# Kernel optimization log

Hardware: AMD Instinct MI355X
Metric: run time of the kernel (lower is better)

Reference implementation:

```python
import jax, jax.numpy as jnp
import numpy as np

NUM_HEADS = 8


def setup_inputs() -> dict:
    key = jax.random.key(0)
    ks = jax.random.split(key, 5)
    B, C, H, W = 2, 256, 64, 64
    # 0.02 scaling keeps logits in a sane range so softmax is not one-hot
    return {
        "x": jax.random.normal(ks[0], (B, C, H, W), dtype=jnp.float32),
        "w_qkv": jax.random.normal(ks[1], (3 * C, C), dtype=jnp.float32) * 0.02,
        "b_qkv": jax.random.normal(ks[2], (3 * C,), dtype=jnp.float32) * 0.02,
        "w_proj": jax.random.normal(ks[3], (C, C), dtype=jnp.float32) * 0.02,
        "b_proj": jax.random.normal(ks[4], (C,), dtype=jnp.float32) * 0.02,
    }


def reference(x, w_qkv, b_qkv, w_proj, b_proj):
    B, C, H, W = x.shape
    N = H * W
    h = NUM_HEADS
    d = C // h
    # 1x1 conv == per-pixel linear: (B,C,H,W) -> (B,3C,H,W)
    qkv = jnp.einsum('oc,bchw->bohw', w_qkv, x) + b_qkv[None, :, None, None]
    qkv = qkv.reshape(B, 3, h, d, N)
    # q,k,v: (B, h, N, d)
    q = jnp.swapaxes(qkv[:, 0], -2, -1)
    k = jnp.swapaxes(qkv[:, 1], -2, -1)
    v = jnp.swapaxes(qkv[:, 2], -2, -1)
    scale = d ** (-0.5)
    attn = jax.nn.softmax(jnp.einsum('bhnd,bhmd->bhnm', q, k) * scale, axis=-1)
    out = jnp.einsum('bhnm,bhmd->bhnd', attn, v)  # (B, h, N, d)
    # faithful to torch: transpose(1,2) -> (B,N,h,d), then row-major reshape to (B,C,H,W)
    out = jnp.swapaxes(out, 1, 2).reshape(B, C, H, W)
    out = jnp.einsum('oc,bchw->bohw', w_proj, out) + b_proj[None, :, None, None]
    return out
```

## Files before the change

### kernel.cpp

```cpp
#include <hip/hip_runtime.h>
#include <hip/hip_bf16.h>


typedef __bf16 bf16;
typedef __bf16 bf16x4 __attribute__((ext_vector_type(4)));
typedef __bf16 bf16x8 __attribute__((ext_vector_type(8)));
typedef float  f32x4  __attribute__((ext_vector_type(4)));
typedef short  s16x4  __attribute__((ext_vector_type(4)));

#if __has_builtin(__builtin_amdgcn_mfma_f32_16x16x16bf16_1k)
#define HAVE_MFMA16 1
#endif

#if __has_builtin(__builtin_amdgcn_exp2f)
#define EXP2(x) __builtin_amdgcn_exp2f(x)
#else
#define EXP2(x) exp2f(x)
#endif

#define NS 4096
#define QSCALE (0.17677669529663687f * 1.4426950408889634f)

static __device__ inline unsigned pack2(float a, float b) {
  union { bf16 h[2]; unsigned u; } v;
  v.h[0] = (bf16)a; v.h[1] = (bf16)b;
  return v.u;
}

__global__ __launch_bounds__(256) void wcvt(
    const float* __restrict__ wq, const float* __restrict__ wp,
    bf16* __restrict__ wqb, bf16* __restrict__ wpb)
{
  const int bid = blockIdx.x, t = threadIdx.x;
  if (bid < 96) {
    const int i = (bid * 256 + t) * 8;
    const float sc = (i < 65536) ? QSCALE : 1.0f;
    f32x4 a = *(const f32x4*)(wq + i);
    f32x4 b = *(const f32x4*)(wq + i + 4);
    bf16x8 o;
#pragma unroll
    for (int j = 0; j < 4; j++) { o[j] = (bf16)(a[j] * sc); o[4 + j] = (bf16)(b[j] * sc); }
    *(bf16x8*)(wqb + i) = o;
  } else {
    const int i = ((bid - 96) * 256 + t) * 8;
    f32x4 a = *(const f32x4*)(wp + i);
    f32x4 b = *(const f32x4*)(wp + i + 4);
    bf16x8 o;
#pragma unroll
    for (int j = 0; j < 4; j++) { o[j] = (bf16)a[j]; o[4 + j] = (bf16)b[j]; }
    *(bf16x8*)(wpb + i) = o;
  }
}

__global__ __launch_bounds__(512) void qkv_fused(
    const float* __restrict__ x, const bf16* __restrict__ wqb,
    const float* __restrict__ bias,
    bf16* __restrict__ qbuf, bf16* __restrict__ kbuf, bf16* __restrict__ vbuf)
{
  __shared__ bf16 As[32 * 264];
  __shared__ bf16 Vt2[2][64 * 40];
  const int n0 = blockIdx.x * 32, b = blockIdx.z ? 1 : blockIdx.y;
  const int bb = blockIdx.y;
  const int t = threadIdx.x;
  const int wv = t >> 6, L = t & 63, quad = L >> 4, lb = L & 15;
  const int grp = wv >> 2, g = wv & 3;
  (void)b;

  {
    unsigned* A32 = (unsigned*)As;
    const int nj = (t & 7) * 4;
    const int cpair = t >> 3;
#pragma unroll
    for (int pass = 0; pass < 2; pass++) {
      const int c = pass * 128 + cpair * 2;
      const float* xr = x + ((size_t)(bb * 256 + c)) * NS + n0 + nj;
      f32x4 va = *(const f32x4*)xr;
      f32x4 vb = *(const f32x4*)(xr + NS);
#pragma unroll
      for (int i = 0; i < 4; i++)
        A32[(nj + i) * 132 + pass * 64 + cpair] = pack2(va[i], vb[i]);
    }
  }
  __syncthreads();

#pragma unroll
  for (int op = 0; op < 6; op++) {
    const int ot = op * 2 + grp;
    const int o = ot * 64 + g * 16 + lb;
    f32x4 acc[2] = {};
#pragma unroll
    for (int ks = 0; ks < 8; ks++) {
      const bf16x8 bfr = *(const bf16x8*)(wqb + (size_t)o * 256 + ks * 32 + quad * 8);
#pragma unroll
      for (int a = 0; a < 2; a++) {
        const bf16x8 afr = *(const bf16x8*)&As[(a * 16 + lb) * 264 + ks * 32 + quad * 8];
        acc[a] = __builtin_amdgcn_mfma_f32_16x16x32_bf16(afr, bfr, acc[a], 0, 0, 0);
      }
    }

    const int comp = ot >> 2;
    const float bv = bias[o] * (comp == 0 ? QSCALE : 1.0f);
    if (comp < 2) {
      bf16* dst = (comp == 0) ? qbuf : kbuf;
      const int hh = (o & 255) >> 5, dd = o & 31;
      const size_t base = ((size_t)bb * 8 + hh) * NS;
#pragma unroll
      for (int a = 0; a < 2; a++)
#pragma unroll
        for (int r = 0; r < 4; r++) {
          const int n = n0 + a * 16 + quad * 4 + r;
          dst[(base + n) * 32 + dd] = (bf16)(acc[a][r] + bv);
        }
    } else {
#pragma unroll
      for (int a = 0; a < 2; a++) {
        bf16x4 pk;
#pragma unroll
        for (int r = 0; r < 4; r++) pk[r] = (bf16)(acc[a][r] + bv);
        *(bf16x4*)&Vt2[grp][(g * 16 + lb) * 40 + a * 16 + quad * 4] = pk;
      }
      __syncthreads();
      {
        const int grp2 = t >> 8, u = t & 255;
        const int row = u >> 2, nc = (u & 3) * 8;
        const int ot2 = op * 2 + grp2;
        const int o2 = ot2 * 64 + row;
        const int hh2 = (o2 & 255) >> 5, dd2 = o2 & 31;
        bf16x8 v = *(const bf16x8*)&Vt2[grp2][row * 40 + nc];
        *(bf16x8*)(vbuf + (((size_t)bb * 8 + hh2) * 32 + dd2) * NS + n0 + nc) = v;
      }
      __syncthreads();
    }
  }
}

#define VT_OFF 2560
#define KV_SZ  (2560 + 32 * 72)

__global__ __launch_bounds__(512) void attn_kernel(
    const bf16* __restrict__ qbuf, const bf16* __restrict__ kbuf,
    const bf16* __restrict__ vbuf, bf16* __restrict__ abuf)
{
  __shared__ bf16 KV[2][KV_SZ];
#ifndef HAVE_MFMA16
  __shared__ bf16 Ps[8][16 * 72];
#endif

  const int qb = blockIdx.x;
  const int bh = blockIdx.y;
  const bf16* Q  = qbuf + (size_t)bh * NS * 32;
  const bf16* K  = kbuf + (size_t)bh * NS * 32;
  const bf16* Vt = vbuf + (size_t)bh * 32 * NS;

  const int t = threadIdx.x;
  const int wv = t >> 6, L = t & 63, quad = L >> 4, lb = L & 15;
  const int qrow = qb * 128 + wv * 16;

  const bf16x8 qfrag = *(const bf16x8*)(Q + (size_t)(qrow + lb) * 32 + quad * 8);

  const int u = t & 255;
  const bool kside = t < 256;
  const int soff = kside ? ((u >> 2) * 40 + (u & 3) * 8)
                         : (VT_OFF + (u >> 3) * 72 + (u & 7) * 8);
  const bf16* gsrc = kside ? (K + (size_t)(u >> 2) * 32 + (u & 3) * 8)
                           : (Vt + (size_t)(u >> 3) * NS + (u & 7) * 8);
  const int gstep = kside ? 64 * 32 : 64;

  bf16x8 reg = *(const bf16x8*)gsrc;

  f32x4 oacc0 = {0.f, 0.f, 0.f, 0.f};
  f32x4 oacc1 = {0.f, 0.f, 0.f, 0.f};
  f32x4 oacc2 = {0.f, 0.f, 0.f, 0.f};
  const f32x4 zero4 = {0.f, 0.f, 0.f, 0.f};
#ifdef HAVE_MFMA16
  const s16x4 ones = {(short)0x3F80, (short)0x3F80, (short)0x3F80, (short)0x3F80};
#else
  float l_i = 0.f;
#endif

#pragma unroll 2
  for (int kt = 0; kt < 64; kt++) {
    const int buf = kt & 1;
    *(bf16x8*)&KV[buf][soff] = reg;
    __syncthreads();
    if (kt < 63) reg = *(const bf16x8*)(gsrc + (size_t)(kt + 1) * gstep);

    f32x4 st[4];
#pragma unroll
    for (int bi = 0; bi < 4; bi++) {
      const bf16x8 kf = *(const bf16x8*)&KV[buf][(bi * 16 + lb) * 40 + quad * 8];
      st[bi] = __builtin_amdgcn_mfma_f32_16x16x32_bf16(kf, qfrag, zero4, 0, 0, 0);
    }

#pragma unroll
    for (int bi = 0; bi < 4; bi++)
#pragma unroll
      for (int r = 0; r < 4; r++) st[bi][r] = EXP2(st[bi][r]);

#ifdef HAVE_MFMA16
#pragma unroll
    for (int bi = 0; bi < 4; bi++) {
      bf16x4 pb;
#pragma unroll
      for (int r = 0; r < 4; r++) pb[r] = (bf16)st[bi][r];
      const s16x4 pf = __builtin_bit_cast(s16x4, pb);
      const s16x4 vf0 = __builtin_bit_cast(s16x4,
          *(const bf16x4*)&KV[buf][VT_OFF + lb * 72 + bi * 16 + quad * 4]);
      const s16x4 vf1 = __builtin_bit_cast(s16x4,
          *(const bf16x4*)&KV[buf][VT_OFF + (16 + lb) * 72 + bi * 16 + quad * 4]);
      oacc0 = __builtin_amdgcn_mfma_f32_16x16x16bf16_1k(pf, vf0, oacc0, 0, 0, 0);
      oacc1 = __builtin_amdgcn_mfma_f32_16x16x16bf16_1k(pf, vf1, oacc1, 0, 0, 0);
      oacc2 = __builtin_amdgcn_mfma_f32_16x16x16bf16_1k(pf, ones, oacc2, 0, 0, 0);
    }
#else
    {
      float ls = 0.f;
#pragma unroll
      for (int bi = 0; bi < 4; bi++)
#pragma unroll
        for (int r = 0; r < 4; r++) ls += st[bi][r];
      l_i += ls;
      bf16* P = &Ps[wv][0];
#pragma unroll
      for (int bi = 0; bi < 4; bi++) {
        bf16x4 pk;
#pragma unroll
        for (int r = 0; r < 4; r++) pk[r] = (bf16)st[bi][r];
        *(bf16x4*)&P[lb * 72 + bi * 16 + quad * 4] = pk;
      }
#pragma unroll
      for (int ch = 0; ch < 2; ch++) {
        const bf16x8 pf  = *(const bf16x8*)&P[lb * 72 + ch * 32 + quad * 8];
        const bf16x8 vf0 = *(const bf16x8*)&KV[buf][VT_OFF + lb * 72 + ch * 32 + quad * 8];
        const bf16x8 vf1 = *(const bf16x8*)&KV[buf][VT_OFF + (16 + lb) * 72 + ch * 32 + quad * 8];
        oacc0 = __builtin_amdgcn_mfma_f32_16x16x32_bf16(pf, vf0, oacc0, 0, 0, 0);
        oacc1 = __builtin_amdgcn_mfma_f32_16x16x32_bf16(pf, vf1, oacc1, 0, 0, 0);
      }
    }
#endif
  }

  const int b_ = bh >> 3;
  const int hh = bh & 7;
#ifndef HAVE_MFMA16
  float lf = l_i;
  lf += __shfl_xor(lf, 16);
  lf += __shfl_xor(lf, 32);
#endif
#pragma unroll
  for (int r = 0; r < 4; r++) {
#ifdef HAVE_MFMA16
    const float lr = oacc2[r];
#else
    const float lr = __shfl(lf, (quad << 4) | (quad * 4 + r));
#endif
#if __has_builtin(__builtin_amdgcn_rcpf)
    const float inv = __builtin_amdgcn_rcpf(lr);
#else
    const float inv = 1.0f / lr;
#endif
    const int n = qrow + quad * 4 + r;
    bf16* dst = abuf + ((size_t)b_ * NS + n) * 256 + hh * 32;
    dst[lb]      = (bf16)(oacc0[r] * inv);
    dst[16 + lb] = (bf16)(oacc1[r] * inv);
  }
}

__global__ __launch_bounds__(256) void proj_fused(
    const bf16* __restrict__ abuf, const bf16* __restrict__ wpb,
    const float* __restrict__ bias, float* __restrict__ out)
{
  __shared__ bf16 Bs[64 * 264];
  const int ch0 = blockIdx.x * 64, o0 = blockIdx.y * 64;
  const int z = blockIdx.z, b = z >> 4, sHi = z & 15;
  const int t = threadIdx.x;
  const int wv = t >> 6, L = t & 63, quad = L >> 4, lb = L & 15;

  {
    const int chj = (t & 7) * 8;
#pragma unroll
    for (int p = 0; p < 8; p++) {
      const int c = p * 32 + (t >> 3);
      bf16x8 v = *(const bf16x8*)(abuf +
          ((size_t)b * NS + (size_t)c * 16 + sHi) * 256 + ch0 + chj);
#pragma unroll
      for (int i = 0; i < 8; i++) Bs[(chj + i) * 264 + c] = v[i];
    }
  }
  __syncthreads();

  f32x4 acc[4] = {};
#pragma unroll
  for (int ks = 0; ks < 8; ks++) {
    const bf16x8 bfr = *(const bf16x8*)&Bs[(wv * 16 + lb) * 264 + ks * 32 + quad * 8];
#pragma unroll
    for (int a = 0; a < 4; a++) {
      const bf16x8 afr = *(const bf16x8*)(wpb +
          (size_t)(o0 + a * 16 + lb) * 256 + ks * 32 + quad * 8);
      acc[a] = __builtin_amdgcn_mfma_f32_16x16x32_bf16(afr, bfr, acc[a], 0, 0, 0);
    }
  }

  const int ch = ch0 + wv * 16 + lb;
#pragma unroll
  for (int a = 0; a < 4; a++)
#pragma unroll
    for (int r = 0; r < 4; r++) {
      const int o = o0 + a * 16 + quad * 4 + r;
      out[((size_t)b * 256 + o) * NS + sHi * 256 + ch] = acc[a][r] + bias[o];
    }
}

extern "C" void kernel_launch(void* const* d_in, const int* in_sizes, int n_in,
                              void* d_out, int out_size, void* d_ws, size_t ws_size,
                              hipStream_t stream) {
  const float* x      = (const float*)d_in[0];
  const float* w_qkv  = (const float*)d_in[1];
  const float* b_qkv  = (const float*)d_in[2];
  const float* w_proj = (const float*)d_in[3];
  const float* b_proj = (const float*)d_in[4];
  float* out = (float*)d_out;

  char* ws = (char*)d_ws;
  const size_t MB = 1024 * 1024;
  bf16* qbuf = (bf16*)(ws);
  bf16* kbuf = (bf16*)(ws + 4 * MB);
  bf16* vbuf = (bf16*)(ws + 8 * MB);
  bf16* abuf = (bf16*)(ws + 12 * MB);
  bf16* wqb  = (bf16*)(ws + 16 * MB);
  bf16* wpb  = (bf16*)(ws + 17 * MB);

  wcvt<<<dim3(128), 256, 0, stream>>>(w_qkv, w_proj, wqb, wpb);
  qkv_fused<<<dim3(128, 2), 512, 0, stream>>>(x, wqb, b_qkv, qbuf, kbuf, vbuf);
  attn_kernel<<<dim3(32, 16), 512, 0, stream>>>(qbuf, kbuf, vbuf, abuf);
  proj_fused<<<dim3(4, 4, 32), 256, 0, stream>>>(abuf, wpb, b_proj, out);
}
```

Before: 157.3 us.

## Split attention KV range across wave groups and double qkv grid

Attention blocks now cover 64 query rows instead of 128, and the two halves of the 8-wave block each process half of the key/value sequence, combining partial outputs and row sums through shared memory at the end. This doubles the attention grid to fill more CUs. The qkv kernel grid gains a z dimension that splits the output-channel tiles between two blocks, and the proj kernel's transposed shared-memory staging is reorganised. The costs are more shared memory, an extra reduction with syncs, and qkv blocks re-staging the x tile twice.

```diff
diff --git a/kernel.cpp b/kernel.cpp
--- a/kernel.cpp
+++ b/kernel.cpp
@@ -59,12 +59,12 @@
 {
   __shared__ bf16 As[32 * 264];
   __shared__ bf16 Vt2[2][64 * 40];
-  const int n0 = blockIdx.x * 32, b = blockIdx.z ? 1 : blockIdx.y;
+  const int n0 = blockIdx.x * 32;
   const int bb = blockIdx.y;
+  const int zz = blockIdx.z;
   const int t = threadIdx.x;
   const int wv = t >> 6, L = t & 63, quad = L >> 4, lb = L & 15;
   const int grp = wv >> 2, g = wv & 3;
-  (void)b;
 
   {
     unsigned* A32 = (unsigned*)As;
@@ -84,7 +84,8 @@
   __syncthreads();
 
 #pragma unroll
-  for (int op = 0; op < 6; op++) {
+  for (int opi = 0; opi < 3; opi++) {
+    const int op = opi * 2 + zz;
     const int ot = op * 2 + grp;
     const int o = ot * 64 + g * 16 + lb;
     f32x4 acc[2] = {};
@@ -141,7 +142,7 @@
     const bf16* __restrict__ qbuf, const bf16* __restrict__ kbuf,
     const bf16* __restrict__ vbuf, bf16* __restrict__ abuf)
 {
-  __shared__ bf16 KV[2][KV_SZ];
+  __shared__ bf16 KV[2][2][KV_SZ];
 #ifndef HAVE_MFMA16
   __shared__ bf16 Ps[8][16 * 72];
 #endif
@@ -154,19 +155,20 @@
 
   const int t = threadIdx.x;
   const int wv = t >> 6, L = t & 63, quad = L >> 4, lb = L & 15;
-  const int qrow = qb * 128 + wv * 16;
+  const int grp = wv >> 2, w = wv & 3;
+  const int qrow = qb * 64 + w * 16;
+  const int kv0 = grp * 2048;
 
   const bf16x8 qfrag = *(const bf16x8*)(Q + (size_t)(qrow + lb) * 32 + quad * 8);
 
   const int u = t & 255;
-  const bool kside = t < 256;
-  const int soff = kside ? ((u >> 2) * 40 + (u & 3) * 8)
-                         : (VT_OFF + (u >> 3) * 72 + (u & 7) * 8);
-  const bf16* gsrc = kside ? (K + (size_t)(u >> 2) * 32 + (u & 3) * 8)
-                           : (Vt + (size_t)(u >> 3) * NS + (u & 7) * 8);
-  const int gstep = kside ? 64 * 32 : 64;
-
-  bf16x8 reg = *(const bf16x8*)gsrc;
+  const int kR = u >> 2, kC = (u & 3) * 8;
+  const int vR = u >> 3, vC = (u & 7) * 8;
+  const bf16* Kg = K + (size_t)(kv0 + kR) * 32 + kC;
+  const bf16* Vg = Vt + (size_t)vR * NS + kv0 + vC;
+
+  bf16x8 kreg = *(const bf16x8*)Kg;
+  bf16x8 vreg = *(const bf16x8*)Vg;
 
   f32x4 oacc0 = {0.f, 0.f, 0.f, 0.f};
   f32x4 oacc1 = {0.f, 0.f, 0.f, 0.f};
@@ -179,16 +181,21 @@
 #endif
 
 #pragma unroll 2
-  for (int kt = 0; kt < 64; kt++) {
+  for (int kt = 0; kt < 32; kt++) {
     const int buf = kt & 1;
-    *(bf16x8*)&KV[buf][soff] = reg;
+    bf16* kv = &KV[grp][buf][0];
+    *(bf16x8*)&kv[kR * 40 + kC] = kreg;
+    *(bf16x8*)&kv[VT_OFF + vR * 72 + vC] = vreg;
     __syncthreads();
-    if (kt < 63) reg = *(const bf16x8*)(gsrc + (size_t)(kt + 1) * gstep);
+    if (kt < 31) {
+      kreg = *(const bf16x8*)(Kg + (size_t)(kt + 1) * 64 * 32);
+      vreg = *(const bf16x8*)(Vg + (size_t)(kt + 1) * 64);
+    }
 
     f32x4 st[4];
 #pragma unroll
     for (int bi = 0; bi < 4; bi++) {
-      const bf16x8 kf = *(const bf16x8*)&KV[buf][(bi * 16 + lb) * 40 + quad * 8];
+      const bf16x8 kf = *(const bf16x8*)&kv[(bi * 16 + lb) * 40 + quad * 8];
       st[bi] = __builtin_amdgcn_mfma_f32_16x16x32_bf16(kf, qfrag, zero4, 0, 0, 0);
     }
 
@@ -205,9 +212,9 @@
       for (int r = 0; r < 4; r++) pb[r] = (bf16)st[bi][r];
       const s16x4 pf = __builtin_bit_cast(s16x4, pb);
       const s16x4 vf0 = __builtin_bit_cast(s16x4,
-          *(const bf16x4*)&KV[buf][VT_OFF + lb * 72 + bi * 16 + quad * 4]);
+          *(const bf16x4*)&kv[VT_OFF + lb * 72 + bi * 16 + quad * 4]);
       const s16x4 vf1 = __builtin_bit_cast(s16x4,
-          *(const bf16x4*)&KV[buf][VT_OFF + (16 + lb) * 72 + bi * 16 + quad * 4]);
+          *(const bf16x4*)&kv[VT_OFF + (16 + lb) * 72 + bi * 16 + quad * 4]);
       oacc0 = __builtin_amdgcn_mfma_f32_16x16x16bf16_1k(pf, vf0, oacc0, 0, 0, 0);
       oacc1 = __builtin_amdgcn_mfma_f32_16x16x16bf16_1k(pf, vf1, oacc1, 0, 0, 0);
       oacc2 = __builtin_amdgcn_mfma_f32_16x16x16bf16_1k(pf, ones, oacc2, 0, 0, 0);
@@ -231,8 +238,8 @@
 #pragma unroll
       for (int ch = 0; ch < 2; ch++) {
         const bf16x8 pf  = *(const bf16x8*)&P[lb * 72 + ch * 32 + quad * 8];
-        const bf16x8 vf0 = *(const bf16x8*)&KV[buf][VT_OFF + lb * 72 + ch * 32 + quad * 8];
-        const bf16x8 vf1 = *(const bf16x8*)&KV[buf][VT_OFF + (16 + lb) * 72 + ch * 32 + quad * 8];
+        const bf16x8 vf0 = *(const bf16x8*)&kv[VT_OFF + lb * 72 + ch * 32 + quad * 8];
+        const bf16x8 vf1 = *(const bf16x8*)&kv[VT_OFF + (16 + lb) * 72 + ch * 32 + quad * 8];
         oacc0 = __builtin_amdgcn_mfma_f32_16x16x32_bf16(pf, vf0, oacc0, 0, 0, 0);
         oacc1 = __builtin_amdgcn_mfma_f32_16x16x32_bf16(pf, vf1, oacc1, 0, 0, 0);
       }
@@ -240,29 +247,46 @@
 #endif
   }
 
-  const int b_ = bh >> 3;
-  const int hh = bh & 7;
 #ifndef HAVE_MFMA16
-  float lf = l_i;
-  lf += __shfl_xor(lf, 16);
-  lf += __shfl_xor(lf, 32);
-#endif
-#pragma unroll
-  for (int r = 0; r < 4; r++) {
-#ifdef HAVE_MFMA16
-    const float lr = oacc2[r];
+  {
+    float lf = l_i;
+    lf += __shfl_xor(lf, 16);
+    lf += __shfl_xor(lf, 32);
+#pragma unroll
+    for (int r = 0; r < 4; r++)
+      oacc2[r] = __shfl(lf, (quad << 4) | (quad * 4 + r));
+  }
+#endif
+
+  float* red = (float*)&KV[0][0][0];
+  __syncthreads();
+  if (grp == 1) {
+    float* dst = red + (size_t)(w * 64 + L) * 12;
+    *(f32x4*)dst = oacc0;
+    *(f32x4*)(dst + 4) = oacc1;
+    *(f32x4*)(dst + 8) = oacc2;
+  }
+  __syncthreads();
+  if (grp == 0) {
+    const float* src = red + (size_t)(w * 64 + L) * 12;
+    oacc0 += *(const f32x4*)src;
+    oacc1 += *(const f32x4*)(src + 4);
+    oacc2 += *(const f32x4*)(src + 8);
+
+    const int b_ = bh >> 3;
+    const int hh = bh & 7;
+#pragma unroll
+    for (int r = 0; r < 4; r++) {
+#if __has_builtin(__builtin_amdgcn_rcpf)
+      const float inv = __builtin_amdgcn_rcpf(oacc2[r]);
 #else
-    const float lr = __shfl(lf, (quad << 4) | (quad * 4 + r));
-#endif
-#if __has_builtin(__builtin_amdgcn_rcpf)
-    const float inv = __builtin_amdgcn_rcpf(lr);
-#else
-    const float inv = 1.0f / lr;
-#endif
-    const int n = qrow + quad * 4 + r;
-    bf16* dst = abuf + ((size_t)b_ * NS + n) * 256 + hh * 32;
-    dst[lb]      = (bf16)(oacc0[r] * inv);
-    dst[16 + lb] = (bf16)(oacc1[r] * inv);
+      const float inv = 1.0f / oacc2[r];
+#endif
+      const int n = qrow + quad * 4 + r;
+      bf16* dst = abuf + ((size_t)b_ * NS + n) * 256 + hh * 32;
+      dst[lb]      = (bf16)(oacc0[r] * inv);
+      dst[16 + lb] = (bf16)(oacc1[r] * inv);
+    }
   }
 }
 
@@ -277,14 +301,19 @@
   const int wv = t >> 6, L = t & 63, quad = L >> 4, lb = L & 15;
 
   {
-    const int chj = (t & 7) * 8;
-#pragma unroll
-    for (int p = 0; p < 8; p++) {
-      const int c = p * 32 + (t >> 3);
-      bf16x8 v = *(const bf16x8*)(abuf +
-          ((size_t)b * NS + (size_t)c * 16 + sHi) * 256 + ch0 + chj);
-#pragma unroll
-      for (int i = 0; i < 8; i++) Bs[(chj + i) * 264 + c] = v[i];
+    const int cl  = t & 63;
+    const int chp = (t >> 6) * 16;
+#pragma unroll
+    for (int p = 0; p < 4; p++) {
+      const int c = p * 64 + cl;
+      const bf16* src = abuf + ((size_t)b * NS + (size_t)c * 16 + sHi) * 256 + ch0 + chp;
+      bf16x8 a0 = *(const bf16x8*)src;
+      bf16x8 a1 = *(const bf16x8*)(src + 8);
+#pragma unroll
+      for (int j = 0; j < 8; j++) {
+        Bs[(chp + j) * 264 + c] = a0[j];
+        Bs[(chp + 8 + j) * 264 + c] = a1[j];
+      }
     }
   }
   __syncthreads();
@@ -331,7 +360,7 @@
   bf16* wpb  = (bf16*)(ws + 17 * MB);
 
   wcvt<<<dim3(128), 256, 0, stream>>>(w_qkv, w_proj, wqb, wpb);
-  qkv_fused<<<dim3(128, 2), 512, 0, stream>>>(x, wqb, b_qkv, qbuf, kbuf, vbuf);
-  attn_kernel<<<dim3(32, 16), 512, 0, stream>>>(qbuf, kbuf, vbuf, abuf);
+  qkv_fused<<<dim3(128, 2, 2), 512, 0, stream>>>(x, wqb, b_qkv, qbuf, kbuf, vbuf);
+  attn_kernel<<<dim3(64, 16), 512, 0, stream>>>(qbuf, kbuf, vbuf, abuf);
   proj_fused<<<dim3(4, 4, 32), 256, 0, stream>>>(abuf, wpb, b_proj, out);
 }
```

Result: no change. 158.7 us (+0.8%).

## Retile QKV projection over output-channel blocks and widen proj staging loads

Applied to the files above, without the earlier changes.

The QKV projection kernel moves from 256 blocks that each loop over all 768 output channels for 32 pixels to 1536 blocks, each computing a 64-pixel by 64-channel tile. This gives far more parallelism and drops the per-iteration V-transpose barriers, but every block reloads and converts its x tile, so x is re-read 12 times. The proj kernel's transposed staging also changes to load 16 bf16 channels per thread per row instead of 8.

```diff
diff --git a/kernel.cpp b/kernel.cpp
--- a/kernel.cpp
+++ b/kernel.cpp
@@ -52,85 +52,75 @@
   }
 }
 
-__global__ __launch_bounds__(512) void qkv_fused(
+__global__ __launch_bounds__(256) void qkv_fused(
     const float* __restrict__ x, const bf16* __restrict__ wqb,
     const float* __restrict__ bias,
     bf16* __restrict__ qbuf, bf16* __restrict__ kbuf, bf16* __restrict__ vbuf)
 {
-  __shared__ bf16 As[32 * 264];
-  __shared__ bf16 Vt2[2][64 * 40];
-  const int n0 = blockIdx.x * 32, b = blockIdx.z ? 1 : blockIdx.y;
-  const int bb = blockIdx.y;
+  __shared__ bf16 As[64 * 264];
+  const int n0 = blockIdx.x * 64, o0 = blockIdx.y * 64, bb = blockIdx.z;
   const int t = threadIdx.x;
   const int wv = t >> 6, L = t & 63, quad = L >> 4, lb = L & 15;
-  const int grp = wv >> 2, g = wv & 3;
-  (void)b;
 
   {
     unsigned* A32 = (unsigned*)As;
-    const int nj = (t & 7) * 4;
-    const int cpair = t >> 3;
-#pragma unroll
-    for (int pass = 0; pass < 2; pass++) {
-      const int c = pass * 128 + cpair * 2;
+    const int nj = (t & 15) * 4;
+#pragma unroll
+    for (int p = 0; p < 8; p++) {
+      const int c = p * 32 + (t >> 4) * 2;
       const float* xr = x + ((size_t)(bb * 256 + c)) * NS + n0 + nj;
       f32x4 va = *(const f32x4*)xr;
       f32x4 vb = *(const f32x4*)(xr + NS);
 #pragma unroll
       for (int i = 0; i < 4; i++)
-        A32[(nj + i) * 132 + pass * 64 + cpair] = pack2(va[i], vb[i]);
+        A32[(nj + i) * 132 + (c >> 1)] = pack2(va[i], vb[i]);
     }
   }
   __syncthreads();
 
-#pragma unroll
-  for (int op = 0; op < 6; op++) {
-    const int ot = op * 2 + grp;
-    const int o = ot * 64 + g * 16 + lb;
-    f32x4 acc[2] = {};
-#pragma unroll
-    for (int ks = 0; ks < 8; ks++) {
-      const bf16x8 bfr = *(const bf16x8*)(wqb + (size_t)o * 256 + ks * 32 + quad * 8);
-#pragma unroll
-      for (int a = 0; a < 2; a++) {
-        const bf16x8 afr = *(const bf16x8*)&As[(a * 16 + lb) * 264 + ks * 32 + quad * 8];
-        acc[a] = __builtin_amdgcn_mfma_f32_16x16x32_bf16(afr, bfr, acc[a], 0, 0, 0);
+  f32x4 acc[4] = {};
+  const int o = o0 + wv * 16 + lb;
+#pragma unroll
+  for (int ks = 0; ks < 8; ks++) {
+    const bf16x8 bfr = *(const bf16x8*)(wqb + (size_t)o * 256 + ks * 32 + quad * 8);
+#pragma unroll
+    for (int a = 0; a < 4; a++) {
+      const bf16x8 afr = *(const bf16x8*)&As[(a * 16 + lb) * 264 + ks * 32 + quad * 8];
+      acc[a] = __builtin_amdgcn_mfma_f32_16x16x32_bf16(afr, bfr, acc[a], 0, 0, 0);
+    }
+  }
+
+  const int comp = o0 >> 8;
+  const float bv = bias[o] * (comp == 0 ? QSCALE : 1.0f);
+  if (comp < 2) {
+    bf16* dst = (comp == 0) ? qbuf : kbuf;
+    const int hh = (o & 255) >> 5, dd = o & 31;
+    const size_t base = ((size_t)bb * 8 + hh) * NS;
+#pragma unroll
+    for (int a = 0; a < 4; a++)
+#pragma unroll
+      for (int r = 0; r < 4; r++) {
+        const int n = n0 + a * 16 + quad * 4 + r;
+        dst[(base + n) * 32 + dd] = (bf16)(acc[a][r] + bv);
       }
-    }
-
-    const int comp = ot >> 2;
-    const float bv = bias[o] * (comp == 0 ? QSCALE : 1.0f);
-    if (comp < 2) {
-      bf16* dst = (comp == 0) ? qbuf : kbuf;
-      const int hh = (o & 255) >> 5, dd = o & 31;
-      const size_t base = ((size_t)bb * 8 + hh) * NS;
-#pragma unroll
-      for (int a = 0; a < 2; a++)
-#pragma unroll
-        for (int r = 0; r < 4; r++) {
-          const int n = n0 + a * 16 + quad * 4 + r;
-          dst[(base + n) * 32 + dd] = (bf16)(acc[a][r] + bv);
-        }
-    } else {
-#pragma unroll
-      for (int a = 0; a < 2; a++) {
-        bf16x4 pk;
-#pragma unroll
-        for (int r = 0; r < 4; r++) pk[r] = (bf16)(acc[a][r] + bv);
-        *(bf16x4*)&Vt2[grp][(g * 16 + lb) * 40 + a * 16 + quad * 4] = pk;
-      }
-      __syncthreads();
-      {
-        const int grp2 = t >> 8, u = t & 255;
-        const int row = u >> 2, nc = (u & 3) * 8;
-        const int ot2 = op * 2 + grp2;
-        const int o2 = ot2 * 64 + row;
-        const int hh2 = (o2 & 255) >> 5, dd2 = o2 & 31;
-        bf16x8 v = *(const bf16x8*)&Vt2[grp2][row * 40 + nc];
-        *(bf16x8*)(vbuf + (((size_t)bb * 8 + hh2) * 32 + dd2) * NS + n0 + nc) = v;
-      }
-      __syncthreads();
-    }
+  } else {
+    __syncthreads();
+    bf16* Vt2 = As;
+#pragma unroll
+    for (int a = 0; a < 4; a++)
+#pragma unroll
+      for (int r = 0; r < 4; r++)
+        Vt2[(wv * 16 + lb) * 72 + a * 16 + quad * 4 + r] = (bf16)(acc[a][r] + bv);
+    __syncthreads();
+    const int row = t & 63;
+    const int o2 = o0 + row;
+    const int hh2 = (o2 & 255) >> 5, dd2 = o2 & 31;
+    const int hc = (t >> 6) * 16;
+    bf16x8 v0 = *(const bf16x8*)&Vt2[row * 72 + hc];
+    bf16x8 v1 = *(const bf16x8*)&Vt2[row * 72 + hc + 8];
+    bf16* vd = vbuf + (((size_t)bb * 8 + hh2) * 32 + dd2) * NS + n0 + hc;
+    *(bf16x8*)vd = v0;
+    *(bf16x8*)(vd + 8) = v1;
   }
 }
 
@@ -277,14 +267,19 @@
   const int wv = t >> 6, L = t & 63, quad = L >> 4, lb = L & 15;
 
   {
-    const int chj = (t & 7) * 8;
-#pragma unroll
-    for (int p = 0; p < 8; p++) {
-      const int c = p * 32 + (t >> 3);
-      bf16x8 v = *(const bf16x8*)(abuf +
-          ((size_t)b * NS + (size_t)c * 16 + sHi) * 256 + ch0 + chj);
-#pragma unroll
-      for (int i = 0; i < 8; i++) Bs[(chj + i) * 264 + c] = v[i];
+    const int cl  = t & 63;
+    const int chp = (t >> 6) * 16;
+#pragma unroll
+    for (int p = 0; p < 4; p++) {
+      const int c = p * 64 + cl;
+      const bf16* src = abuf + ((size_t)b * NS + (size_t)c * 16 + sHi) * 256 + ch0 + chp;
+      bf16x8 a0 = *(const bf16x8*)src;
+      bf16x8 a1 = *(const bf16x8*)(src + 8);
+#pragma unroll
+      for (int j = 0; j < 8; j++) {
+        Bs[(chp + j) * 264 + c] = a0[j];
+        Bs[(chp + 8 + j) * 264 + c] = a1[j];
+      }
     }
   }
   __syncthreads();
@@ -331,7 +326,7 @@
   bf16* wpb  = (bf16*)(ws + 17 * MB);
 
   wcvt<<<dim3(128), 256, 0, stream>>>(w_qkv, w_proj, wqb, wpb);
-  qkv_fused<<<dim3(128, 2), 512, 0, stream>>>(x, wqb, b_qkv, qbuf, kbuf, vbuf);
+  qkv_fused<<<dim3(64, 12, 2), 256, 0, stream>>>(x, wqb, b_qkv, qbuf, kbuf, vbuf);
   attn_kernel<<<dim3(32, 16), 512, 0, stream>>>(qbuf, kbuf, vbuf, abuf);
   proj_fused<<<dim3(4, 4, 32), 256, 0, stream>>>(abuf, wpb, b_proj, out);
 }
```

Result: faster. 153.2 us (-2.6%).
